# Kernel optimization log

Measured on AMD Instinct MI355X. Metric: run time of the kernel, lower is better.

Reference implementation:

```python
import jax, jax.numpy as jnp
import numpy as np
import math

B, NX, NY = 2, 2048, 2048
CX, CY = 1024, 1024
KEY_CH, VAL_CH, HEADS = 1024, 1024, 16


def setup_inputs() -> dict:
    key = jax.random.key(0)
    ks = jax.random.split(key, 10)
    s = lambda fan_in: 1.0 / math.sqrt(fan_in)
    inp = {
        "x": jax.random.normal(ks[0], (B, NX, CX), dtype=jnp.float32),
        "y": jax.random.normal(ks[1], (B, NY, CY), dtype=jnp.float32),
        "Wq": jax.random.uniform(ks[2], (CX, KEY_CH), jnp.float32, -s(CX), s(CX)),
        "bq": jax.random.uniform(ks[3], (KEY_CH,), jnp.float32, -s(CX), s(CX)),
        "Wk": jax.random.uniform(ks[4], (CY, KEY_CH), jnp.float32, -s(CY), s(CY)),
        "bk": jax.random.uniform(ks[5], (KEY_CH,), jnp.float32, -s(CY), s(CY)),
        "Wv": jax.random.uniform(ks[6], (CY, VAL_CH), jnp.float32, -s(CY), s(CY)),
        "bv": jax.random.uniform(ks[7], (VAL_CH,), jnp.float32, -s(CY), s(CY)),
        "Wo": jax.random.uniform(ks[8], (VAL_CH, CX), jnp.float32, -s(VAL_CH), s(VAL_CH)),
        "bo": jax.random.uniform(ks[9], (CX,), jnp.float32, -s(VAL_CH), s(VAL_CH)),
    }
    return inp


def reference(x, y, Wq, bq, Wk, bk, Wv, bv, Wo, bo):
    Bx, Nx, _ = x.shape
    By, Ny, _ = y.shape
    dk = KEY_CH // HEADS
    dv = VAL_CH // HEADS
    # projections
    q = (x @ Wq + bq).reshape(Bx, Nx, HEADS, dk)  # contiguous head slices == reshape
    k = (y @ Wk + bk).reshape(By, Ny, HEADS, dk)
    v = (y @ Wv + bv).reshape(By, Ny, HEADS, dv)
    # NOTE: original scales by 1/sqrt(Ny) (sequence length), not 1/sqrt(dk)
    scores = jnp.einsum("bnhd,bmhd->bhnm", q, k) / jnp.sqrt(jnp.float32(Ny))
    attn = jax.nn.softmax(scores, axis=-1)
    out = jnp.einsum("bhnm,bmhd->bnhd", attn, v).reshape(Bx, Nx, VAL_CH)
    out = jax.nn.relu(out @ Wo + bo)
    # dropout(p=0.2) is identity in eval mode
    return out
```

## Files before the change

### kernel.cpp

```cpp
#include <hip/hip_runtime.h>
#include <hip/hip_bf16.h>

typedef __bf16 bf16;
typedef __attribute__((ext_vector_type(8))) __bf16 bf16x8;
typedef __attribute__((ext_vector_type(4))) __bf16 bf16x4;
typedef __attribute__((ext_vector_type(4))) float f32x4;
typedef __attribute__((ext_vector_type(16))) float f32x16;
typedef __attribute__((ext_vector_type(4))) unsigned int u32x4;

__device__ __forceinline__ void gload_lds16(const void* g, void* l) {
  __builtin_amdgcn_global_load_lds((const __attribute__((address_space(1))) void*)g,
                                   (__attribute__((address_space(3))) void*)l, 16, 0, 0);
}

__device__ __forceinline__ float exp2_fast(float x) {
  float r;
  asm("v_exp_f32 %0, %1" : "=v"(r) : "v"(x));
  return r;
}

__device__ __forceinline__ unsigned pk2(float a, float b) {
  unsigned short lo = __builtin_bit_cast(unsigned short, (bf16)a);
  unsigned short hi = __builtin_bit_cast(unsigned short, (bf16)b);
  return (unsigned)lo | ((unsigned)hi << 16);
}

__global__ __launch_bounds__(256) void cvt2_kernel(const float4* __restrict__ a,
                                                   const float4* __restrict__ b,
                                                   bf16x4* __restrict__ oa,
                                                   bf16x4* __restrict__ ob, int n4) {
  int i = blockIdx.x * 256 + threadIdx.x;
  const float4* in = a; bf16x4* out = oa;
  if (i >= n4) { in = b; out = ob; i -= n4; }
  float4 v = in[i];
  bf16x4 o;
  o[0] = (bf16)v.x; o[1] = (bf16)v.y; o[2] = (bf16)v.z; o[3] = (bf16)v.w;
  out[i] = o;
}

__global__ __launch_bounds__(256) void wtrans_kernel(
    const float* __restrict__ W0, const float* __restrict__ W1,
    const float* __restrict__ W2, const float* __restrict__ W3,
    bf16* __restrict__ T0, bf16* __restrict__ T1,
    bf16* __restrict__ T2, bf16* __restrict__ T3) {
  const float* W; bf16* T;
  switch (blockIdx.z) {
    case 0: W = W0; T = T0; break;
    case 1: W = W1; T = T1; break;
    case 2: W = W2; T = T2; break;
    default: W = W3; T = T3; break;
  }
  __shared__ float t[32][33];
  int tx = threadIdx.x, ty = threadIdx.y;
  int bn = blockIdx.x * 32, bk = blockIdx.y * 32;
#pragma unroll
  for (int i = 0; i < 32; i += 8)
    t[ty + i][tx] = W[(size_t)(bk + ty + i) * 1024 + bn + tx];
  __syncthreads();
#pragma unroll
  for (int i = 0; i < 32; i += 8)
    T[(size_t)(bn + ty + i) * 1024 + bk + tx] = (bf16)t[tx][ty + i];
}

__global__ __launch_bounds__(256) void gemm_qkv(
    const bf16* __restrict__ xb, const bf16* __restrict__ yb,
    const bf16* __restrict__ Wqt, const bf16* __restrict__ Wkt, const bf16* __restrict__ Wvt,
    const float* __restrict__ bq, const float* __restrict__ bk, const float* __restrict__ bv,
    bf16* __restrict__ Qb, bf16* __restrict__ Kb, bf16* __restrict__ Vtb) {
  constexpr int K = 1024;
  constexpr float QSCALE = (float)(1.4426950408889634 / 45.254833995939045);
  __shared__ bf16 As[2][128 * 32];
  __shared__ bf16 Bs[2][128 * 32];
  const int z = blockIdx.z;
  const bf16* A  = (z == 0) ? xb : yb;
  const bf16* Bt = (z == 0) ? Wqt : (z == 1) ? Wkt : Wvt;
  const float* bias = (z == 0) ? bq : (z == 1) ? bk : bv;

  const int tid = threadIdx.x;
  const int wave = tid >> 6, lane = tid & 63;
  const int g = lane >> 4, r15 = lane & 15;
  const int m0 = blockIdx.x * 128, n0 = blockIdx.y * 128;
  const int wr = wave >> 1, wc = wave & 1;

  f32x4 acc[4][4] = {};

  const int c0 = tid, c1 = tid + 256;
  const int row0 = c0 >> 2, ch0 = c0 & 3;
  const int row1 = c1 >> 2, ch1 = c1 & 3;

  auto stage = [&](int buf, int k0) {
    gload_lds16(A  + (size_t)(m0 + row0) * K + k0 + ch0 * 8, (char*)As[buf] + c0 * 16);
    gload_lds16(Bt + (size_t)(n0 + row0) * K + k0 + ch0 * 8, (char*)Bs[buf] + c0 * 16);
    gload_lds16(A  + (size_t)(m0 + row1) * K + k0 + ch1 * 8, (char*)As[buf] + c1 * 16);
    gload_lds16(Bt + (size_t)(n0 + row1) * K + k0 + ch1 * 8, (char*)Bs[buf] + c1 * 16);
  };

  stage(0, 0);
  __syncthreads();
  int cur = 0;
  for (int t = 0; t < K / 32; ++t) {
    if (t + 1 < K / 32) stage(cur ^ 1, (t + 1) * 32);
    bf16x8 af[4], bfr[4];
#pragma unroll
    for (int mi = 0; mi < 4; ++mi)
      af[mi] = *(const bf16x8*)((const char*)As[cur] + ((wr * 64 + mi * 16 + r15) * 64 + g * 16));
#pragma unroll
    for (int nj = 0; nj < 4; ++nj)
      bfr[nj] = *(const bf16x8*)((const char*)Bs[cur] + ((wc * 64 + nj * 16 + r15) * 64 + g * 16));
#pragma unroll
    for (int mi = 0; mi < 4; ++mi)
#pragma unroll
      for (int nj = 0; nj < 4; ++nj)
        acc[mi][nj] = __builtin_amdgcn_mfma_f32_16x16x32_bf16(af[mi], bfr[nj], acc[mi][nj], 0, 0, 0);
    __syncthreads();
    cur ^= 1;
  }

  const float scl = (z == 0) ? QSCALE : 1.0f;
#pragma unroll
  for (int mi = 0; mi < 4; ++mi) {
#pragma unroll
    for (int nj = 0; nj < 4; ++nj) {
      int row = m0 + wr * 64 + mi * 16 + g * 4;
      int col = n0 + wc * 64 + nj * 16 + r15;
      float bv_ = bias[col];
      if (z < 2) {
        bf16* C = (z == 0) ? Qb : Kb;
#pragma unroll
        for (int r = 0; r < 4; ++r)
          C[(size_t)(row + r) * 1024 + col] = (bf16)((acc[mi][nj][r] + bv_) * scl);
      } else {
        int b = row >> 11, n = row & 2047;
        bf16x4 pkv;
#pragma unroll
        for (int r = 0; r < 4; ++r)
          pkv[r] = (bf16)(acc[mi][nj][r] + bv_);
        *(bf16x4*)(Vtb + ((size_t)b * 1024 + col) * 2048 + n) = pkv;
      }
    }
  }
}

__global__ __launch_bounds__(256) void gemm_out(
    const bf16* __restrict__ A, const bf16* __restrict__ Bt,
    const float* __restrict__ bias, float* __restrict__ C) {
  constexpr int K = 1024;
  __shared__ bf16 As[2][128 * 32];
  __shared__ bf16 Bs[2][64 * 32];
  const int tid = threadIdx.x;
  const int wave = tid >> 6, lane = tid & 63;
  const int g = lane >> 4, r15 = lane & 15;
  const int m0 = blockIdx.x * 128, n0 = blockIdx.y * 64;
  const int wr = wave >> 1, wc = wave & 1;

  f32x4 acc[4][2] = {};

  const int c0 = tid, c1 = tid + 256;
  const int row0 = c0 >> 2, ch0 = c0 & 3;
  const int row1 = c1 >> 2, ch1 = c1 & 3;

  auto stage = [&](int buf, int k0) {
    gload_lds16(A + (size_t)(m0 + row0) * K + k0 + ch0 * 8, (char*)As[buf] + c0 * 16);
    gload_lds16(A + (size_t)(m0 + row1) * K + k0 + ch1 * 8, (char*)As[buf] + c1 * 16);
    gload_lds16(Bt + (size_t)(n0 + row0) * K + k0 + ch0 * 8, (char*)Bs[buf] + c0 * 16);
  };

  stage(0, 0);
  __syncthreads();
  int cur = 0;
  for (int t = 0; t < K / 32; ++t) {
    if (t + 1 < K / 32) stage(cur ^ 1, (t + 1) * 32);
    bf16x8 af[4], bfr[2];
#pragma unroll
    for (int mi = 0; mi < 4; ++mi)
      af[mi] = *(const bf16x8*)((const char*)As[cur] + ((wr * 64 + mi * 16 + r15) * 64 + g * 16));
#pragma unroll
    for (int nj = 0; nj < 2; ++nj)
      bfr[nj] = *(const bf16x8*)((const char*)Bs[cur] + ((wc * 32 + nj * 16 + r15) * 64 + g * 16));
#pragma unroll
    for (int mi = 0; mi < 4; ++mi)
#pragma unroll
      for (int nj = 0; nj < 2; ++nj)
        acc[mi][nj] = __builtin_amdgcn_mfma_f32_16x16x32_bf16(af[mi], bfr[nj], acc[mi][nj], 0, 0, 0);
    __syncthreads();
    cur ^= 1;
  }

#pragma unroll
  for (int mi = 0; mi < 4; ++mi)
#pragma unroll
    for (int nj = 0; nj < 2; ++nj) {
      int row = m0 + wr * 64 + mi * 16 + g * 4;
      int col = n0 + wc * 32 + nj * 16 + r15;
      float bv_ = bias[col];
#pragma unroll
      for (int r = 0; r < 4; ++r)
        C[(size_t)(row + r) * 1024 + col] = fmaxf(acc[mi][nj][r] + bv_, 0.0f);
    }
}

__global__ __launch_bounds__(128, 2) void attn_kernel(
    const bf16* __restrict__ Q, const bf16* __restrict__ Kin,
    const bf16* __restrict__ Vt, bf16* __restrict__ Oa) {
  __shared__ bf16 Ks[2][64 * 64];
  __shared__ bf16 Vs[2][64 * 64];
  const int tid = threadIdx.x;
  const int wave = tid >> 6, lane = tid & 63;
  const int q5 = lane & 31, h = lane >> 5;

  int i = blockIdx.y * 32 + blockIdx.x;
  int xcd = i & 7, slot = i >> 3;
  int bh = xcd * 4 + (slot >> 5), qt = slot & 31;
  int b = bh >> 4, hd = bh & 15;

  const bf16* Qg = Q + ((size_t)b * 2048 + qt * 64 + wave * 32) * 1024 + hd * 64;
  const bf16* Kg = Kin + (size_t)b * 2048 * 1024 + hd * 64;
  const bf16* Vg = Vt + ((size_t)b * 1024 + hd * 64) * 2048;

  bf16x8 qf[4];
#pragma unroll
  for (int ks = 0; ks < 4; ++ks)
    qf[ks] = *(const bf16x8*)(Qg + (size_t)q5 * 1024 + ks * 16 + h * 8);

  f32x16 o0 = {}, o1 = {};
  float ls = 0.0f;

  auto stage = [&](int buf, int kv0) {
#pragma unroll
    for (int ii = 0; ii < 4; ++ii) {
      int c = tid + ii * 128;
      int row = c >> 3, ch = (c & 7) ^ (row & 7);
      gload_lds16(Kg + (size_t)(kv0 + row) * 1024 + ch * 8, (char*)Ks[buf] + c * 16);
      gload_lds16(Vg + (size_t)row * 2048 + kv0 + ch * 8, (char*)Vs[buf] + c * 16);
    }
  };

  stage(0, 0);
  __syncthreads();
  int cur = 0;

  for (int t = 0; t < 32; ++t) {
    if (t < 31) stage(cur ^ 1, (t + 1) * 64);

    f32x16 s0 = {}, s1 = {};
    __builtin_amdgcn_s_setprio(1);
#pragma unroll
    for (int ks = 0; ks < 4; ++ks) {
      int chk = ((2 * ks + h) ^ (q5 & 7)) * 16;
      bf16x8 k0 = *(const bf16x8*)((const char*)Ks[cur] + q5 * 128 + chk);
      bf16x8 k1 = *(const bf16x8*)((const char*)Ks[cur] + (q5 + 32) * 128 + chk);
      s0 = __builtin_amdgcn_mfma_f32_32x32x16_bf16(k0, qf[ks], s0, 0, 0, 0);
      s1 = __builtin_amdgcn_mfma_f32_32x32x16_bf16(k1, qf[ks], s1, 0, 0, 0);
    }
    __builtin_amdgcn_s_setprio(0);

    unsigned pw0[4][2], pw1[4][2];
#pragma unroll
    for (int g4 = 0; g4 < 4; ++g4) {
      float e0 = exp2_fast(s0[g4 * 4 + 0]), e1 = exp2_fast(s0[g4 * 4 + 1]);
      float e2 = exp2_fast(s0[g4 * 4 + 2]), e3 = exp2_fast(s0[g4 * 4 + 3]);
      float f0 = exp2_fast(s1[g4 * 4 + 0]), f1 = exp2_fast(s1[g4 * 4 + 1]);
      float f2 = exp2_fast(s1[g4 * 4 + 2]), f3 = exp2_fast(s1[g4 * 4 + 3]);
      ls += (e0 + e1) + (e2 + e3) + (f0 + f1) + (f2 + f3);
      pw0[g4][0] = pk2(e0, e1); pw0[g4][1] = pk2(e2, e3);
      pw1[g4][0] = pk2(f0, f1); pw1[g4][1] = pk2(f2, f3);
    }

    __builtin_amdgcn_s_setprio(1);
#pragma unroll
    for (int ks = 0; ks < 4; ++ks) {
      const unsigned (*pw)[2] = (ks < 2) ? pw0 : pw1;
      const int base = (ks & 1) * 2;
      unsigned a0 = pw[base][0], a1 = pw[base][1];
      unsigned b0 = pw[base + 1][0], b1 = pw[base + 1][1];
      unsigned s0w = h ? a0 : b0, s1w = h ? a1 : b1;
      unsigned r0 = __shfl_xor(s0w, 32), r1 = __shfl_xor(s1w, 32);
      unsigned o0w = h ? b0 : a0, o1w = h ? b1 : a1;
      u32x4 w;
      w[0] = h ? r0 : o0w; w[1] = h ? r1 : o1w;
      w[2] = h ? o0w : r0; w[3] = h ? o1w : r1;
      bf16x8 pa = __builtin_bit_cast(bf16x8, w);
      int chk = ((2 * ks + h) ^ (q5 & 7)) * 16;
      bf16x8 v0 = *(const bf16x8*)((const char*)Vs[cur] + q5 * 128 + chk);
      bf16x8 v1 = *(const bf16x8*)((const char*)Vs[cur] + (q5 + 32) * 128 + chk);
      o0 = __builtin_amdgcn_mfma_f32_32x32x16_bf16(pa, v0, o0, 0, 0, 0);
      o1 = __builtin_amdgcn_mfma_f32_32x32x16_bf16(pa, v1, o1, 0, 0, 0);
    }
    __builtin_amdgcn_s_setprio(0);

    __syncthreads();
    cur ^= 1;
  }

  ls += __shfl_xor(ls, 32);
  float inv = __builtin_amdgcn_rcpf(ls);

#pragma unroll
  for (int g4 = 0; g4 < 4; ++g4)
#pragma unroll
    for (int r = 0; r < 4; ++r) {
      int qr = g4 * 8 + 4 * h + r;
      float il = __shfl(inv, qr);
      size_t row = (size_t)b * 2048 + qt * 64 + wave * 32 + qr;
      bf16* dst = Oa + row * 1024 + hd * 64;
      dst[q5]      = (bf16)(o0[g4 * 4 + r] * il);
      dst[q5 + 32] = (bf16)(o1[g4 * 4 + r] * il);
    }
}

extern "C" void kernel_launch(void* const* d_in, const int* in_sizes, int n_in,
                              void* d_out, int out_size, void* d_ws, size_t ws_size,
                              hipStream_t stream) {
  (void)in_sizes; (void)n_in; (void)out_size; (void)ws_size;
  const float* x  = (const float*)d_in[0];
  const float* y  = (const float*)d_in[1];
  const float* Wq = (const float*)d_in[2];
  const float* bq = (const float*)d_in[3];
  const float* Wk = (const float*)d_in[4];
  const float* bk = (const float*)d_in[5];
  const float* Wv = (const float*)d_in[6];
  const float* bv = (const float*)d_in[7];
  const float* Wo = (const float*)d_in[8];
  const float* bo = (const float*)d_in[9];

  char* ws = (char*)d_ws;
  bf16* xb  = (bf16*)(ws + 0);
  bf16* yb  = (bf16*)(ws + 8388608);
  bf16* Qb  = (bf16*)(ws + 16777216);
  bf16* Kb  = (bf16*)(ws + 25165824);
  bf16* Vtb = (bf16*)(ws + 33554432);
  bf16* Oab = (bf16*)(ws + 41943040);
  bf16* Wqt = (bf16*)(ws + 50331648);
  bf16* Wkt = (bf16*)(ws + 52428800);
  bf16* Wvt = (bf16*)(ws + 54525952);
  bf16* Wot = (bf16*)(ws + 56623104);

  const int n4 = 4096 * 1024 / 4;
  cvt2_kernel<<<2 * n4 / 256, 256, 0, stream>>>((const float4*)x, (const float4*)y,
                                                (bf16x4*)xb, (bf16x4*)yb, n4);
  wtrans_kernel<<<dim3(32, 32, 4), dim3(32, 8), 0, stream>>>(Wq, Wk, Wv, Wo, Wqt, Wkt, Wvt, Wot);
  gemm_qkv<<<dim3(32, 8, 3), 256, 0, stream>>>(xb, yb, Wqt, Wkt, Wvt, bq, bk, bv, Qb, Kb, Vtb);
  attn_kernel<<<dim3(32, 32), dim3(128), 0, stream>>>(Qb, Kb, Vtb, Oab);
  gemm_out<<<dim3(32, 16), 256, 0, stream>>>(Oab, Wot, bo, (float*)d_out);
}
```

Before: 141.6 us.

## Split attention KV across waves, use permlane swap and packed cvt, merge prep kernels

```diff
diff --git a/kernel.cpp b/kernel.cpp
--- a/kernel.cpp
+++ b/kernel.cpp
@@ -19,47 +19,54 @@
   return r;
 }
 
-__device__ __forceinline__ unsigned pk2(float a, float b) {
-  unsigned short lo = __builtin_bit_cast(unsigned short, (bf16)a);
-  unsigned short hi = __builtin_bit_cast(unsigned short, (bf16)b);
-  return (unsigned)lo | ((unsigned)hi << 16);
-}
-
-__global__ __launch_bounds__(256) void cvt2_kernel(const float4* __restrict__ a,
-                                                   const float4* __restrict__ b,
-                                                   bf16x4* __restrict__ oa,
-                                                   bf16x4* __restrict__ ob, int n4) {
-  int i = blockIdx.x * 256 + threadIdx.x;
-  const float4* in = a; bf16x4* out = oa;
-  if (i >= n4) { in = b; out = ob; i -= n4; }
-  float4 v = in[i];
-  bf16x4 o;
-  o[0] = (bf16)v.x; o[1] = (bf16)v.y; o[2] = (bf16)v.z; o[3] = (bf16)v.w;
-  out[i] = o;
-}
-
-__global__ __launch_bounds__(256) void wtrans_kernel(
+__device__ __forceinline__ unsigned cvtpk(float lo, float hi) {
+  unsigned r;
+  asm("v_cvt_pk_bf16_f32 %0, %1, %2" : "=v"(r) : "v"(lo), "v"(hi));
+  return r;
+}
+
+__device__ __forceinline__ void plswap(unsigned& a, unsigned& b) {
+  asm("v_permlane32_swap_b32 %0, %1" : "+v"(a), "+v"(b));
+}
+
+__global__ __launch_bounds__(256) void cvtw_kernel(
+    const float* __restrict__ x, const float* __restrict__ y,
+    bf16* __restrict__ xb, bf16* __restrict__ yb,
     const float* __restrict__ W0, const float* __restrict__ W1,
     const float* __restrict__ W2, const float* __restrict__ W3,
     bf16* __restrict__ T0, bf16* __restrict__ T1,
     bf16* __restrict__ T2, bf16* __restrict__ T3) {
-  const float* W; bf16* T;
-  switch (blockIdx.z) {
-    case 0: W = W0; T = T0; break;
-    case 1: W = W1; T = T1; break;
-    case 2: W = W2; T = T2; break;
-    default: W = W3; T = T3; break;
-  }
   __shared__ float t[32][33];
-  int tx = threadIdx.x, ty = threadIdx.y;
-  int bn = blockIdx.x * 32, bk = blockIdx.y * 32;
-#pragma unroll
-  for (int i = 0; i < 32; i += 8)
-    t[ty + i][tx] = W[(size_t)(bk + ty + i) * 1024 + bn + tx];
-  __syncthreads();
-#pragma unroll
-  for (int i = 0; i < 32; i += 8)
-    T[(size_t)(bn + ty + i) * 1024 + bk + tx] = (bf16)t[tx][ty + i];
+  const int bid = blockIdx.x, tid = threadIdx.x;
+  if (bid < 4096) {
+    const int z = bid >> 10, rem = bid & 1023;
+    const int bx = rem & 31, by = rem >> 5;
+    const float* W; bf16* T;
+    switch (z) {
+      case 0: W = W0; T = T0; break;
+      case 1: W = W1; T = T1; break;
+      case 2: W = W2; T = T2; break;
+      default: W = W3; T = T3; break;
+    }
+    const int tx = tid & 31, ty = tid >> 5;
+    const int bn = bx * 32, bk = by * 32;
+#pragma unroll
+    for (int i = 0; i < 32; i += 8)
+      t[ty + i][tx] = W[(size_t)(bk + ty + i) * 1024 + bn + tx];
+    __syncthreads();
+#pragma unroll
+    for (int i = 0; i < 32; i += 8)
+      T[(size_t)(bn + ty + i) * 1024 + bk + tx] = (bf16)t[tx][ty + i];
+  } else {
+    const int n4 = 1048576;
+    int i = (bid - 4096) * 256 + tid;
+    const float4* in = (const float4*)x; bf16x4* out = (bf16x4*)xb;
+    if (i >= n4) { in = (const float4*)y; out = (bf16x4*)yb; i -= n4; }
+    float4 v = in[i];
+    bf16x4 o;
+    o[0] = (bf16)v.x; o[1] = (bf16)v.y; o[2] = (bf16)v.z; o[3] = (bf16)v.w;
+    out[i] = o;
+  }
 }
 
 __global__ __launch_bounds__(256) void gemm_qkv(
@@ -204,8 +211,9 @@
     const bf16* __restrict__ Vt, bf16* __restrict__ Oa) {
   __shared__ bf16 Ks[2][64 * 64];
   __shared__ bf16 Vs[2][64 * 64];
+  __shared__ float lsh[2][2][32];
   const int tid = threadIdx.x;
-  const int wave = tid >> 6, lane = tid & 63;
+  const int w = tid >> 6, lane = tid & 63;
   const int q5 = lane & 31, h = lane >> 5;
 
   int i = blockIdx.y * 32 + blockIdx.x;
@@ -213,25 +221,28 @@
   int bh = xcd * 4 + (slot >> 5), qt = slot & 31;
   int b = bh >> 4, hd = bh & 15;
 
-  const bf16* Qg = Q + ((size_t)b * 2048 + qt * 64 + wave * 32) * 1024 + hd * 64;
+  const bf16* Qg = Q + ((size_t)b * 2048 + qt * 64) * 1024 + hd * 64;
   const bf16* Kg = Kin + (size_t)b * 2048 * 1024 + hd * 64;
   const bf16* Vg = Vt + ((size_t)b * 1024 + hd * 64) * 2048;
 
-  bf16x8 qf[4];
-#pragma unroll
-  for (int ks = 0; ks < 4; ++ks)
-    qf[ks] = *(const bf16x8*)(Qg + (size_t)q5 * 1024 + ks * 16 + h * 8);
-
-  f32x16 o0 = {}, o1 = {};
-  float ls = 0.0f;
+  bf16x8 qf[2][4];
+#pragma unroll
+  for (int qb = 0; qb < 2; ++qb)
+#pragma unroll
+    for (int ks = 0; ks < 4; ++ks)
+      qf[qb][ks] = *(const bf16x8*)(Qg + (size_t)(qb * 32 + q5) * 1024 + ks * 16 + h * 8);
+
+  f32x16 o[2][2] = {};
+  float ls[2] = {};
 
   auto stage = [&](int buf, int kv0) {
 #pragma unroll
     for (int ii = 0; ii < 4; ++ii) {
       int c = tid + ii * 128;
-      int row = c >> 3, ch = (c & 7) ^ (row & 7);
-      gload_lds16(Kg + (size_t)(kv0 + row) * 1024 + ch * 8, (char*)Ks[buf] + c * 16);
-      gload_lds16(Vg + (size_t)row * 2048 + kv0 + ch * 8, (char*)Vs[buf] + c * 16);
+      int row = c >> 3;
+      int sl = (c & 7) ^ (row & 7) ^ ((row >> 3) & 1);
+      gload_lds16(Kg + (size_t)(kv0 + row) * 1024 + sl * 8, (char*)Ks[buf] + c * 16);
+      gload_lds16(Vg + (size_t)row * 2048 + kv0 + sl * 8, (char*)Vs[buf] + c * 16);
     }
   };
 
@@ -239,52 +250,55 @@
   __syncthreads();
   int cur = 0;
 
+  const int krow = w * 32 + q5;
+  const int kswz = (krow & 7) ^ ((krow >> 3) & 1);
+
   for (int t = 0; t < 32; ++t) {
     if (t < 31) stage(cur ^ 1, (t + 1) * 64);
 
-    f32x16 s0 = {}, s1 = {};
+    f32x16 s[2] = {};
     __builtin_amdgcn_s_setprio(1);
 #pragma unroll
     for (int ks = 0; ks < 4; ++ks) {
-      int chk = ((2 * ks + h) ^ (q5 & 7)) * 16;
-      bf16x8 k0 = *(const bf16x8*)((const char*)Ks[cur] + q5 * 128 + chk);
-      bf16x8 k1 = *(const bf16x8*)((const char*)Ks[cur] + (q5 + 32) * 128 + chk);
-      s0 = __builtin_amdgcn_mfma_f32_32x32x16_bf16(k0, qf[ks], s0, 0, 0, 0);
-      s1 = __builtin_amdgcn_mfma_f32_32x32x16_bf16(k1, qf[ks], s1, 0, 0, 0);
+      bf16x8 kf = *(const bf16x8*)((const char*)Ks[cur] + krow * 128 + (((2 * ks + h) ^ kswz) << 4));
+      s[0] = __builtin_amdgcn_mfma_f32_32x32x16_bf16(kf, qf[0][ks], s[0], 0, 0, 0);
+      s[1] = __builtin_amdgcn_mfma_f32_32x32x16_bf16(kf, qf[1][ks], s[1], 0, 0, 0);
     }
     __builtin_amdgcn_s_setprio(0);
 
-    unsigned pw0[4][2], pw1[4][2];
-#pragma unroll
-    for (int g4 = 0; g4 < 4; ++g4) {
-      float e0 = exp2_fast(s0[g4 * 4 + 0]), e1 = exp2_fast(s0[g4 * 4 + 1]);
-      float e2 = exp2_fast(s0[g4 * 4 + 2]), e3 = exp2_fast(s0[g4 * 4 + 3]);
-      float f0 = exp2_fast(s1[g4 * 4 + 0]), f1 = exp2_fast(s1[g4 * 4 + 1]);
-      float f2 = exp2_fast(s1[g4 * 4 + 2]), f3 = exp2_fast(s1[g4 * 4 + 3]);
-      ls += (e0 + e1) + (e2 + e3) + (f0 + f1) + (f2 + f3);
-      pw0[g4][0] = pk2(e0, e1); pw0[g4][1] = pk2(e2, e3);
-      pw1[g4][0] = pk2(f0, f1); pw1[g4][1] = pk2(f2, f3);
+    unsigned u[2][8];
+#pragma unroll
+    for (int qb = 0; qb < 2; ++qb) {
+      float e[16];
+#pragma unroll
+      for (int j = 0; j < 16; ++j) e[j] = exp2_fast(s[qb][j]);
+      ls[qb] += ((((e[0] + e[1]) + (e[2] + e[3])) + ((e[4] + e[5]) + (e[6] + e[7]))) +
+                 (((e[8] + e[9]) + (e[10] + e[11])) + ((e[12] + e[13]) + (e[14] + e[15]))));
+#pragma unroll
+      for (int p = 0; p < 8; ++p) u[qb][p] = cvtpk(e[2 * p], e[2 * p + 1]);
+      plswap(u[qb][0], u[qb][2]); plswap(u[qb][1], u[qb][3]);
+      plswap(u[qb][4], u[qb][6]); plswap(u[qb][5], u[qb][7]);
     }
 
     __builtin_amdgcn_s_setprio(1);
 #pragma unroll
-    for (int ks = 0; ks < 4; ++ks) {
-      const unsigned (*pw)[2] = (ks < 2) ? pw0 : pw1;
-      const int base = (ks & 1) * 2;
-      unsigned a0 = pw[base][0], a1 = pw[base][1];
-      unsigned b0 = pw[base + 1][0], b1 = pw[base + 1][1];
-      unsigned s0w = h ? a0 : b0, s1w = h ? a1 : b1;
-      unsigned r0 = __shfl_xor(s0w, 32), r1 = __shfl_xor(s1w, 32);
-      unsigned o0w = h ? b0 : a0, o1w = h ? b1 : a1;
-      u32x4 w;
-      w[0] = h ? r0 : o0w; w[1] = h ? r1 : o1w;
-      w[2] = h ? o0w : r0; w[3] = h ? o1w : r1;
-      bf16x8 pa = __builtin_bit_cast(bf16x8, w);
-      int chk = ((2 * ks + h) ^ (q5 & 7)) * 16;
-      bf16x8 v0 = *(const bf16x8*)((const char*)Vs[cur] + q5 * 128 + chk);
-      bf16x8 v1 = *(const bf16x8*)((const char*)Vs[cur] + (q5 + 32) * 128 + chk);
-      o0 = __builtin_amdgcn_mfma_f32_32x32x16_bf16(pa, v0, o0, 0, 0, 0);
-      o1 = __builtin_amdgcn_mfma_f32_32x32x16_bf16(pa, v1, o1, 0, 0, 0);
+    for (int j = 0; j < 2; ++j) {
+      const int db = w ^ j;
+      const int vrow0 = db * 32 + q5;
+      const int vswz = (vrow0 & 7) ^ ((vrow0 >> 3) & 1);
+#pragma unroll
+      for (int kap = 0; kap < 2; ++kap) {
+        bf16x8 vb = *(const bf16x8*)((const char*)Vs[cur] + vrow0 * 128 +
+                                     (((4 * w + 2 * kap + h) ^ vswz) << 4));
+#pragma unroll
+        for (int qb = 0; qb < 2; ++qb) {
+          u32x4 uw;
+          uw[0] = u[qb][4 * kap + 0]; uw[1] = u[qb][4 * kap + 1];
+          uw[2] = u[qb][4 * kap + 2]; uw[3] = u[qb][4 * kap + 3];
+          bf16x8 pa = __builtin_bit_cast(bf16x8, uw);
+          o[qb][j] = __builtin_amdgcn_mfma_f32_32x32x16_bf16(pa, vb, o[qb][j], 0, 0, 0);
+        }
+      }
     }
     __builtin_amdgcn_s_setprio(0);
 
@@ -292,20 +306,31 @@
     cur ^= 1;
   }
 
-  ls += __shfl_xor(ls, 32);
-  float inv = __builtin_amdgcn_rcpf(ls);
-
-#pragma unroll
-  for (int g4 = 0; g4 < 4; ++g4)
-#pragma unroll
-    for (int r = 0; r < 4; ++r) {
-      int qr = g4 * 8 + 4 * h + r;
-      float il = __shfl(inv, qr);
-      size_t row = (size_t)b * 2048 + qt * 64 + wave * 32 + qr;
-      bf16* dst = Oa + row * 1024 + hd * 64;
-      dst[q5]      = (bf16)(o0[g4 * 4 + r] * il);
-      dst[q5 + 32] = (bf16)(o1[g4 * 4 + r] * il);
-    }
+  ls[0] += __shfl_xor(ls[0], 32);
+  ls[1] += __shfl_xor(ls[1], 32);
+  if (h == 0) { lsh[w][0][q5] = ls[0]; lsh[w][1][q5] = ls[1]; }
+
+  float* osh = (float*)Ks;
+#pragma unroll
+  for (int qb = 0; qb < 2; ++qb)
+    *(f32x16*)(osh + ((w * 2 + qb) * 64 + lane) * 16) = o[qb][1];
+  __syncthreads();
+
+#pragma unroll
+  for (int qb = 0; qb < 2; ++qb) {
+    float lt = ls[qb] + lsh[1 - w][qb][q5];
+    float iv = __builtin_amdgcn_rcpf(lt);
+    f32x16 p = *(const f32x16*)(osh + (((1 - w) * 2 + qb) * 64 + lane) * 16);
+#pragma unroll
+    for (int g4 = 0; g4 < 4; ++g4)
+#pragma unroll
+      for (int r = 0; r < 4; ++r) {
+        int qr = g4 * 8 + 4 * h + r;
+        float il = __shfl(iv, qr);
+        size_t row = (size_t)b * 2048 + qt * 64 + qb * 32 + qr;
+        Oa[row * 1024 + hd * 64 + w * 32 + q5] = (bf16)((o[qb][0][g4 * 4 + r] + p[g4 * 4 + r]) * il);
+      }
+  }
 }
 
 extern "C" void kernel_launch(void* const* d_in, const int* in_sizes, int n_in,
@@ -335,10 +360,7 @@
   bf16* Wvt = (bf16*)(ws + 54525952);
   bf16* Wot = (bf16*)(ws + 56623104);
 
-  const int n4 = 4096 * 1024 / 4;
-  cvt2_kernel<<<2 * n4 / 256, 256, 0, stream>>>((const float4*)x, (const float4*)y,
-                                                (bf16x4*)xb, (bf16x4*)yb, n4);
-  wtrans_kernel<<<dim3(32, 32, 4), dim3(32, 8), 0, stream>>>(Wq, Wk, Wv, Wo, Wqt, Wkt, Wvt, Wot);
+  cvtw_kernel<<<12288, 256, 0, stream>>>(x, y, xb, yb, Wq, Wk, Wv, Wo, Wqt, Wkt, Wvt, Wot);
   gemm_qkv<<<dim3(32, 8, 3), 256, 0, stream>>>(xb, yb, Wqt, Wkt, Wvt, bq, bk, bv, Qb, Kb, Vtb);
   attn_kernel<<<dim3(32, 32), dim3(128), 0, stream>>>(Qb, Kb, Vtb, Oab);
   gemm_out<<<dim3(32, 16), 256, 0, stream>>>(Oab, Wot, bo, (float*)d_out);
```

After: 131.6 us. 1.08x faster.
